# Kernel optimization log

Hardware: AMD Instinct MI355X
Metric: run time of the kernel (lower is better)

The kernel has to match this reference:

```python
import jax, jax.numpy as jnp
import numpy as np

NTOKEN, NINP, NHID, NLAYERS = 33278, 400, 1150, 3


def _lstm_scan(x_seq, h0, c0, Wih, Whh, bih, bhh):
    # x_seq: [T,B,in], h0/c0: [B,H]; PyTorch gate order i,f,g,o
    def step(carry, x):
        h, c = carry
        gates = x @ Wih.T + bih + h @ Whh.T + bhh  # [B,4H]
        i, f, g, o = jnp.split(gates, 4, axis=-1)
        c = jax.nn.sigmoid(f) * c + jax.nn.sigmoid(i) * jnp.tanh(g)
        h = jax.nn.sigmoid(o) * jnp.tanh(c)
        return (h, c), h
    (hT, cT), hs = jax.lax.scan(step, (h0, c0), x_seq)
    return hs, hT, cT


def _causal_attention(hs):
    # hs: [T,B,H]; dot-product attention of h_t over h_{0..t} (causal)
    T = hs.shape[0]
    scores = jnp.einsum('tbh,sbh->bts', hs, hs)  # [B,T,T]
    mask = jnp.tril(jnp.ones((T, T), dtype=bool))
    scores = jnp.where(mask[None, :, :], scores, -1e30)
    attn = jax.nn.softmax(scores, axis=-1)
    return jnp.einsum('bts,sbh->tbh', attn, hs)


def setup_inputs() -> dict:
    key = jax.random.key(0)
    ks = jax.random.split(key, 24)
    T, B = 100, 64
    inp = {
        'input': jax.random.randint(ks[0], (T, B), 0, NTOKEN),
        'input2': jax.random.randint(ks[1], (T, B), 0, NTOKEN),
        'h0': jnp.zeros((1, B, NHID)), 'c0': jnp.zeros((1, B, NHID)),
        'h1': jnp.zeros((1, B, NHID)), 'c1': jnp.zeros((1, B, NHID)),
        'h2': jnp.zeros((1, B, NHID)), 'c2': jnp.zeros((1, B, NHID)),
    }
    inp['emb_W'] = jax.random.uniform(ks[2], (NTOKEN, NINP), minval=-0.1, maxval=0.1)
    in_sizes = [2 * NINP, NHID, NHID]
    for l in range(NLAYERS):
        s = 1.0 / np.sqrt(NHID)
        inp[f'W_ih{l}'] = jax.random.uniform(ks[3 + 4 * l], (4 * NHID, in_sizes[l]), minval=-s, maxval=s)
        inp[f'W_hh{l}'] = jax.random.uniform(ks[4 + 4 * l], (4 * NHID, NHID), minval=-s, maxval=s)
        inp[f'b_ih{l}'] = jax.random.uniform(ks[5 + 4 * l], (4 * NHID,), minval=-s, maxval=s)
        inp[f'b_hh{l}'] = jax.random.uniform(ks[6 + 4 * l], (4 * NHID,), minval=-s, maxval=s)
    inp['dec_W'] = jax.random.uniform(ks[20], (NTOKEN, NHID), minval=-0.1, maxval=0.1)
    inp['dec_b'] = jnp.zeros((NTOKEN,))
    return inp


def reference(input, input2, h0, c0, h1, c1, h2, c2, emb_W,
              W_ih0, W_hh0, b_ih0, b_hh0,
              W_ih1, W_hh1, b_ih1, b_hh1,
              W_ih2, W_hh2, b_ih2, b_hh2,
              dec_W, dec_b):
    # eval mode: all dropouts are identity
    emb = jnp.concatenate([emb_W[input], emb_W[input2]], axis=-1)  # [T,B,2*ninp]
    x = emb
    hcs = [(h0[0], c0[0]), (h1[0], c1[0]), (h2[0], c2[0])]
    params = [(W_ih0, W_hh0, b_ih0, b_hh0), (W_ih1, W_hh1, b_ih1, b_hh1), (W_ih2, W_hh2, b_ih2, b_hh2)]
    for l in range(NLAYERS):
        hs, hT, cT = _lstm_scan(x, hcs[l][0], hcs[l][1], *params[l])
        if l == NLAYERS - 1:
            out = _causal_attention(hs)  # attention only on last layer
        else:
            x = hs
    T, B, H = out.shape
    decoded = out.reshape(T * B, H) @ dec_W.T + dec_b  # [T*B, ntoken]
    return decoded
```

## Files before the change

kernel.cpp:

```cpp
#include <hip/hip_runtime.h>
#include <stdint.h>

typedef unsigned short ushort_t;
typedef __bf16 bf16x8 __attribute__((ext_vector_type(8)));
typedef float f32x4 __attribute__((ext_vector_type(4)));

__device__ __forceinline__ float b2f(ushort_t u) {
  union { unsigned u; float f; } v; v.u = ((unsigned)u) << 16; return v.f;
}
__device__ __forceinline__ ushort_t f2b(float f) {
  union { float f; unsigned u; } v; v.f = f;
  unsigned r = (v.u + 0x7FFFu + ((v.u >> 16) & 1u)) >> 16;
  return (ushort_t)r;
}

__device__ __forceinline__ float sigm(float x)     { return 1.f / (1.f + __expf(-x)); }
__device__ __forceinline__ float tanhfast(float x) { return 1.f - 2.f / (1.f + __expf(2.f * x)); }

__device__ __forceinline__ void store_short_wt(ushort_t* p, ushort_t v) {
  asm volatile("global_store_short %0, %1, off sc0 sc1"
               :: "v"(p), "v"((unsigned)v) : "memory");
}
__device__ __forceinline__ void store_uint_wt(unsigned* p, unsigned v) {
  asm volatile("global_store_dword %0, %1, off sc0 sc1"
               :: "v"(p), "v"(v) : "memory");
}

__device__ __forceinline__ void gload_lds16(const void* g, void* lds) {
  auto l3 = reinterpret_cast<__attribute__((address_space(3))) unsigned*>(
      reinterpret_cast<uintptr_t>(lds));
  __builtin_amdgcn_global_load_lds(reinterpret_cast<const unsigned*>(g), l3, 16, 0, 0);
}

template <bool F32OUT>
__global__ __launch_bounds__(512) void gemm_bt(
    const ushort_t* __restrict__ A, const ushort_t* __restrict__ B,
    void* __restrict__ Cv,
    const float* __restrict__ bias0, const float* __restrict__ bias1,
    int lda, int ldb, long ldc, int Kpad, int N)
{
  __shared__ alignas(16) ushort_t As[256 * 32];
  __shared__ alignas(16) ushort_t Bs[256 * 32];
  const int tid = threadIdx.x;
  const int w = tid >> 6, l = tid & 63;
  const int wr = w >> 2, wc = w & 3;

  unsigned nwg = gridDim.x * gridDim.y;
  unsigned wg = blockIdx.y * gridDim.x + blockIdx.x;
  {
    unsigned q = nwg >> 3, r = nwg & 7u;
    unsigned xcd = wg & 7u, idx = wg >> 3;
    wg = (xcd < r ? xcd * (q + 1) : r * (q + 1) + (xcd - r) * q) + idx;
  }
  const long m0 = (long)(wg % gridDim.x) * 256;
  const long n0 = (long)(wg / gridDim.x) * 256;

  const int lrow = l & 15, hi = l >> 4, lk = hi * 8;

  f32x4 acc[8][4] = {};

  const int c0 = tid, c1 = tid + 512;
  const int r0 = c0 >> 2, g0 = (c0 & 3) * 8;
  const int r1 = c1 >> 2, g1 = (c1 & 3) * 8;

  for (int k0 = 0; k0 < Kpad; k0 += 32) {
    gload_lds16(A + (m0 + r0) * lda + k0 + g0, As + c0 * 8);
    gload_lds16(A + (m0 + r1) * lda + k0 + g1, As + c1 * 8);
    gload_lds16(B + (n0 + r0) * ldb + k0 + g0, Bs + c0 * 8);
    gload_lds16(B + (n0 + r1) * ldb + k0 + g1, Bs + c1 * 8);
    __syncthreads();

    bf16x8 af[8], bfr[4];
#pragma unroll
    for (int mi = 0; mi < 8; mi++)
      af[mi] = *(const bf16x8*)(As + (wr * 128 + mi * 16 + lrow) * 32 + lk);
#pragma unroll
    for (int ni = 0; ni < 4; ni++)
      bfr[ni] = *(const bf16x8*)(Bs + (wc * 64 + ni * 16 + lrow) * 32 + lk);
#pragma unroll
    for (int mi = 0; mi < 8; mi++)
#pragma unroll
      for (int ni = 0; ni < 4; ni++)
        acc[mi][ni] = __builtin_amdgcn_mfma_f32_16x16x32_bf16(af[mi], bfr[ni], acc[mi][ni], 0, 0, 0);
    __syncthreads();
  }

  const int rbase = hi * 4;
#pragma unroll
  for (int ni = 0; ni < 4; ni++) {
    int gcol = (int)n0 + wc * 64 + ni * 16 + lrow;
    if (gcol < N) {
      float badd = 0.f;
      if (bias0) badd += bias0[gcol];
      if (bias1) badd += bias1[gcol];
#pragma unroll
      for (int mi = 0; mi < 8; mi++) {
#pragma unroll
        for (int r = 0; r < 4; r++) {
          long grow = m0 + wr * 128 + mi * 16 + rbase + r;
          float v = acc[mi][ni][r] + badd;
          if (F32OUT) ((float*)Cv)[grow * ldc + gcol] = v;
          else        ((ushort_t*)Cv)[grow * ldc + gcol] = f2b(v);
        }
      }
    }
  }
}

__global__ __launch_bounds__(256) void lstm_layer(
    ushort_t* __restrict__ hs,
    const ushort_t* __restrict__ G,
    const ushort_t* __restrict__ Whh,
    const float* __restrict__ c_in,
    unsigned* __restrict__ flags)
{
  extern __shared__ ushort_t Bsh[];
  const int tid = threadIdx.x;
  const int w = tid >> 6, l = tid & 63;
  const int us = blockIdx.x;
  const int lrow = l & 15, hi = l >> 4, lk = hi * 8;
  const int u = us * 16 + lrow;
  const int usafe = (u < 1150) ? u : 0;
  const int row0 = w * 16 + hi * 4;
  const int x7 = lrow & 7;
  const int start = us >> 1;

  for (int ci = tid; ci < 9216; ci += 256) {
    int gate = ci / 2304;
    int rem  = ci - gate * 2304;
    int row  = rem / 144;
    int c    = rem - row * 144;
    bf16x8 v = *(const bf16x8*)(Whh + ((long)(gate * 1150 + us * 16 + row)) * 1152 + c * 8);
    *(bf16x8*)(Bsh + (((gate * 16 + row) * 144) + (c ^ (row & 7))) * 8) = v;
  }
  const ushort_t* Bg0 = Bsh + ((0 * 16 + lrow) * 144) * 8;
  const ushort_t* Bg1 = Bsh + ((1 * 16 + lrow) * 144) * 8;
  const ushort_t* Bg2 = Bsh + ((2 * 16 + lrow) * 144) * 8;
  const ushort_t* Bg3 = Bsh + ((3 * 16 + lrow) * 144) * 8;

  f32x4 cc = {};
  if (u < 1150) {
#pragma unroll
    for (int r = 0; r < 4; ++r) cc[r] = c_in[(row0 + r) * 1150 + u];
  }
  __syncthreads();

  const int s1 = l, s2 = 64 + (l & 7);

  for (int t = 0; t < 100; ++t) {
    ushort_t gvv[16];
    {
      const ushort_t* gp = G + ((long)t * 64 + row0) * 4608 + usafe;
#pragma unroll
      for (int r = 0; r < 4; ++r)
#pragma unroll
        for (int g = 0; g < 4; ++g)
          gvv[r * 4 + g] = gp[(long)r * 4608 + g * 1150];
    }

    if (t > 0) {
      if (w == 0) {
        const unsigned tt = (unsigned)t;
        unsigned f1 = (s1 == us) ? tt :
            __hip_atomic_load(flags + (s1 << 5), __ATOMIC_RELAXED, __HIP_MEMORY_SCOPE_AGENT);
        unsigned f2 = (s2 == us) ? tt :
            __hip_atomic_load(flags + (s2 << 5), __ATOMIC_RELAXED, __HIP_MEMORY_SCOPE_AGENT);
        unsigned long long p1 = __ballot(f1 >= tt);
        unsigned long long p2 = __ballot(f2 >= tt);
        while ((p1 & p2) != ~0ull) {
          __builtin_amdgcn_s_sleep(8);
          if (!((p1 >> l) & 1))
            f1 = __hip_atomic_load(flags + (s1 << 5), __ATOMIC_RELAXED, __HIP_MEMORY_SCOPE_AGENT);
          if (!((p2 >> l) & 1))
            f2 = __hip_atomic_load(flags + (s2 << 5), __ATOMIC_RELAXED, __HIP_MEMORY_SCOPE_AGENT);
          p1 = __ballot(f1 >= tt);
          p2 = __ballot(f2 >= tt);
        }
      }
      __syncthreads();
      asm volatile("" ::: "memory");
    }

    const ushort_t* hp = hs + (long)t * 73728 + (long)(w * 16 + lrow) * 1152 + lk;
    f32x4 a0 = {}, a1 = {}, a2 = {}, a3 = {};
#pragma unroll 4
    for (int i = 0; i < 36; ++i) {
      int kc = start + i; if (kc >= 36) kc -= 36;
      bf16x8 a = *(const bf16x8*)(hp + kc * 32);
      int pc8 = ((kc * 4 + hi) ^ x7) * 8;
      a0 = __builtin_amdgcn_mfma_f32_16x16x32_bf16(a, *(const bf16x8*)(Bg0 + pc8), a0, 0, 0, 0);
      a1 = __builtin_amdgcn_mfma_f32_16x16x32_bf16(a, *(const bf16x8*)(Bg1 + pc8), a1, 0, 0, 0);
      a2 = __builtin_amdgcn_mfma_f32_16x16x32_bf16(a, *(const bf16x8*)(Bg2 + pc8), a2, 0, 0, 0);
      a3 = __builtin_amdgcn_mfma_f32_16x16x32_bf16(a, *(const bf16x8*)(Bg3 + pc8), a3, 0, 0, 0);
    }

    if (u < 1150) {
#pragma unroll
      for (int r = 0; r < 4; ++r) {
        float iv = a0[r] + b2f(gvv[r * 4 + 0]);
        float fv = a1[r] + b2f(gvv[r * 4 + 1]);
        float gg = a2[r] + b2f(gvv[r * 4 + 2]);
        float ov = a3[r] + b2f(gvv[r * 4 + 3]);
        float cn = sigm(fv) * cc[r] + sigm(iv) * tanhfast(gg);
        cc[r] = cn;
        float hv = sigm(ov) * tanhfast(cn);
        store_short_wt(hs + (long)(t + 1) * 73728 + (long)(row0 + r) * 1152 + u, f2b(hv));
      }
    }

    if (t != 99) {
      asm volatile("s_waitcnt vmcnt(0)" ::: "memory");
      __syncthreads();
      if (tid == 0) store_uint_wt(flags + (us << 5), (unsigned)(t + 1));
    }
  }
}

__global__ __launch_bounds__(256) void attn_kernel(
    const ushort_t* __restrict__ hs2,
    ushort_t* __restrict__ outp)
{
  __shared__ float qf[1152];
  __shared__ float sc[104];
  __shared__ float sinv;
  const int rowi = blockIdx.x;
  const int t = rowi >> 6, b = rowi & 63;
  const int tid = threadIdx.x;
  const int w = tid >> 6, l = tid & 63;

  const ushort_t* q = hs2 + (long)rowi * 1152;
  for (int c = tid; c < 1150; c += 256) qf[c] = b2f(q[c]);
  __syncthreads();

  for (int s = w; s <= t; s += 4) {
    const ushort_t* k = hs2 + (long)(s * 64 + b) * 1152;
    float p = 0.f;
    for (int h = l; h < 1150; h += 64) p += qf[h] * b2f(k[h]);
    for (int off = 32; off; off >>= 1) p += __shfl_down(p, off);
    if (l == 0) sc[s] = p;
  }
  __syncthreads();

  if (w == 0) {
    float m = -1e30f;
    for (int s = l; s <= t; s += 64) m = fmaxf(m, sc[s]);
    for (int off = 32; off; off >>= 1) m = fmaxf(m, __shfl_down(m, off));
    m = __shfl(m, 0);
    float sum = 0.f;
    for (int s = l; s <= t; s += 64) { float e = __expf(sc[s] - m); sc[s] = e; sum += e; }
    for (int off = 32; off; off >>= 1) sum += __shfl_down(sum, off);
    if (l == 0) sinv = 1.f / sum;
  }
  __syncthreads();

  const float si = sinv;
  for (int h = tid; h < 1150; h += 256) {
    float a = 0.f;
    for (int s = 0; s <= t; s++) a += sc[s] * b2f(hs2[(long)(s * 64 + b) * 1152 + h]);
    outp[(long)rowi * 1152 + h] = f2b(a * si);
  }
  if (tid < 2) outp[(long)rowi * 1152 + 1150 + tid] = 0;
}

__global__ void embed_kernel(const int* __restrict__ in1, const int* __restrict__ in2,
                             const float* __restrict__ emb, ushort_t* __restrict__ x0)
{
  int rowi = blockIdx.x;
  int l = threadIdx.x;
  long r1 = (long)in1[rowi] * 400, r2 = (long)in2[rowi] * 400;
  ushort_t* d = x0 + (long)rowi * 800;
  for (int c = l; c < 800; c += 64)
    d[c] = f2b(c < 400 ? emb[r1 + c] : emb[r2 + c - 400]);
}

__global__ void pad_convert(const float* __restrict__ in, ushort_t* __restrict__ out,
                            int R, int Cin, int total, int Cp)
{
  int idx = blockIdx.x * 256 + threadIdx.x;
  if (idx >= total) return;
  int r = idx / Cp, c = idx - r * Cp;
  float v = (r < R && c < Cin) ? in[(long)r * Cin + c] : 0.f;
  out[idx] = f2b(v);
}

__global__ void init_state(const float* __restrict__ h_in,
                           ushort_t* __restrict__ hs, unsigned* __restrict__ flags)
{
  int idx = blockIdx.x * 256 + threadIdx.x;
  if (idx < 72 * 32) flags[idx] = 0u;
  if (idx < 64 * 1152) {
    int b = idx / 1152, c = idx - b * 1152;
    hs[idx] = (c < 1150) ? f2b(h_in[b * 1150 + c]) : (ushort_t)0;
  }
  if (idx < 100 * 128) {
    int t = idx >> 7, r = idx & 127, b = r >> 1, k = r & 1;
    hs[(long)(t + 1) * 73728 + b * 1152 + 1150 + k] = 0;
  }
}

extern "C" void kernel_launch(void* const* d_in, const int* in_sizes, int n_in,
                              void* d_out, int out_size, void* d_ws, size_t ws_size,
                              hipStream_t stream) {
  (void)in_sizes; (void)n_in; (void)out_size; (void)ws_size;
  const int* input  = (const int*)d_in[0];
  const int* input2 = (const int*)d_in[1];
  const float* h_in[3] = {(const float*)d_in[2], (const float*)d_in[4], (const float*)d_in[6]};
  const float* c_in[3] = {(const float*)d_in[3], (const float*)d_in[5], (const float*)d_in[7]};
  const float* emb_W = (const float*)d_in[8];
  const float* W_ih[3] = {(const float*)d_in[9],  (const float*)d_in[13], (const float*)d_in[17]};
  const float* W_hh[3] = {(const float*)d_in[10], (const float*)d_in[14], (const float*)d_in[18]};
  const float* b_ih[3] = {(const float*)d_in[11], (const float*)d_in[15], (const float*)d_in[19]};
  const float* b_hh[3] = {(const float*)d_in[12], (const float*)d_in[16], (const float*)d_in[20]};
  const float* dec_W = (const float*)d_in[21];
  const float* dec_b = (const float*)d_in[22];
  float* out = (float*)d_out;

  hipFuncSetAttribute((const void*)lstm_layer,
                      hipFuncAttributeMaxDynamicSharedMemorySize, 147456);

  char* base = (char*)d_ws;
  size_t off = 0;
  auto walloc = [&](size_t bytes) { char* r = base + off; off += (bytes + 255) & ~(size_t)255; return r; };
  ushort_t* decWp = (ushort_t*)walloc(33280ull * 1152 * 2);
  ushort_t* attnB = (ushort_t*)walloc(6400ull * 1152 * 2);
  unsigned* flags = (unsigned*)walloc(72 * 128 + 256);

  char* ob = (char*)d_out;
  ushort_t* G   = (ushort_t*)(ob + 0);
  ushort_t* x0  = (ushort_t*)(ob + 58982400);
  ushort_t* Wp  = (ushort_t*)(ob + 69222400);
  ushort_t* Whp = (ushort_t*)(ob + 79839232);
  ushort_t* hsA = (ushort_t*)(ob + 90456064);
  ushort_t* hsB = (ushort_t*)(ob + 105349120);

  embed_kernel<<<6400, 64, 0, stream>>>(input, input2, emb_W, x0);

  ushort_t* hcur[3] = {hsA, hsB, hsA};
  const ushort_t* X = x0;
  int lda = 800, Kp = 800;
  for (int lyr = 0; lyr < 3; lyr++) {
    if (lyr == 0) {
      int tot = 4608 * 800;
      pad_convert<<<(tot + 255) / 256, 256, 0, stream>>>(W_ih[0], Wp, 4600, 800, tot, 800);
    } else {
      int tot = 4608 * 1152;
      pad_convert<<<(tot + 255) / 256, 256, 0, stream>>>(W_ih[lyr], Wp, 4600, 1150, tot, 1152);
    }
    {
      int tot = 4608 * 1152;
      pad_convert<<<(tot + 255) / 256, 256, 0, stream>>>(W_hh[lyr], Whp, 4600, 1150, tot, 1152);
    }
    gemm_bt<false><<<dim3(25, 18), 512, 0, stream>>>(X, Wp, (void*)G, b_ih[lyr], b_hh[lyr],
                                                     lda, Kp, 4608L, Kp, 4600);
    init_state<<<288, 256, 0, stream>>>(h_in[lyr], hcur[lyr], flags);
    lstm_layer<<<72, 256, 147456, stream>>>(hcur[lyr], G, Whp, c_in[lyr], flags);
    X = hcur[lyr] + 73728;
    lda = 1152; Kp = 1152;
  }

  attn_kernel<<<6400, 256, 0, stream>>>(hsA + 73728, attnB);

  {
    int tot = 33280 * 1152;
    pad_convert<<<(tot + 255) / 256, 256, 0, stream>>>(dec_W, decWp, 33278, 1150, tot, 1152);
  }

  gemm_bt<true><<<dim3(25, 130), 512, 0, stream>>>(attnB, decWp, (void*)out, dec_b, nullptr,
                                                   1152, 1152, 33278L, 1152, 33278);
}
```

Measured before the change: 3.997 ms.

## Fuse three LSTM layers into one wavefront-pipelined persistent kernel

Replaces three sequential per-layer LSTM launches (each preceded by an input-projection GEMM) with a single persistent kernel of 216 blocks, 72 per layer. Layers 1 and 2 compute the input projection inline by streaming W_ih rows from global memory, and each waits on per-timestep flags from the layer below, so the three layers run as a diagonal wavefront. This removes the two layer-1/2 input GEMMs and the serialization between layers. In exchange it doubles the MFMA work per step for upper layers, reads uncached W_ih from global/L2 every step, and needs all 216 blocks co-resident with 144KB LDS each to avoid deadlock.

```diff
diff --git a/kernel.cpp b/kernel.cpp
--- a/kernel.cpp
+++ b/kernel.cpp
@@ -107,23 +107,44 @@
   }
 }
 
-__global__ __launch_bounds__(256) void lstm_layer(
-    ushort_t* __restrict__ hs,
-    const ushort_t* __restrict__ G,
-    const ushort_t* __restrict__ Whh,
-    const float* __restrict__ c_in,
+__global__ __launch_bounds__(256) void lstm_fused3(
+    ushort_t* __restrict__ hs0, ushort_t* __restrict__ hs1, ushort_t* __restrict__ hs2,
+    const ushort_t* __restrict__ G0,
+    const ushort_t* __restrict__ Whp0, const ushort_t* __restrict__ Whp1,
+    const ushort_t* __restrict__ Whp2,
+    const ushort_t* __restrict__ Wip1, const ushort_t* __restrict__ Wip2,
+    const float* __restrict__ c0, const float* __restrict__ c1, const float* __restrict__ c2,
+    const float* __restrict__ bi1, const float* __restrict__ bh1,
+    const float* __restrict__ bi2, const float* __restrict__ bh2,
     unsigned* __restrict__ flags)
 {
   extern __shared__ ushort_t Bsh[];
   const int tid = threadIdx.x;
   const int w = tid >> 6, l = tid & 63;
-  const int us = blockIdx.x;
+  const int L  = blockIdx.x / 72;
+  const int us = blockIdx.x % 72;
   const int lrow = l & 15, hi = l >> 4, lk = hi * 8;
   const int u = us * 16 + lrow;
   const int usafe = (u < 1150) ? u : 0;
   const int row0 = w * 16 + hi * 4;
   const int x7 = lrow & 7;
   const int start = us >> 1;
+
+  ushort_t* hsL = (L == 0) ? hs0 : (L == 1) ? hs1 : hs2;
+  const ushort_t* hsP = (L == 1) ? hs0 : hs1;
+  const ushort_t* Whh = (L == 0) ? Whp0 : (L == 1) ? Whp1 : Whp2;
+  const ushort_t* Wih = (L == 1) ? Wip1 : Wip2;
+  const float* cin = (L == 0) ? c0 : (L == 1) ? c1 : c2;
+  unsigned* fown  = flags + L * 2304;
+  unsigned* fprev = flags + (L - 1) * 2304;
+
+  float bias4[4] = {0.f, 0.f, 0.f, 0.f};
+  if (L > 0) {
+    const float* bi = (L == 1) ? bi1 : bi2;
+    const float* bh = (L == 1) ? bh1 : bh2;
+#pragma unroll
+    for (int g = 0; g < 4; ++g) bias4[g] = bi[g * 1150 + usafe] + bh[g * 1150 + usafe];
+  }
 
   for (int ci = tid; ci < 9216; ci += 256) {
     int gate = ci / 2304;
@@ -138,19 +159,42 @@
   const ushort_t* Bg2 = Bsh + ((2 * 16 + lrow) * 144) * 8;
   const ushort_t* Bg3 = Bsh + ((3 * 16 + lrow) * 144) * 8;
 
+  const ushort_t* wi0 = Wih + ((long)(0 * 1150 + us * 16 + lrow)) * 1152 + lk;
+  const ushort_t* wi1 = Wih + ((long)(1 * 1150 + us * 16 + lrow)) * 1152 + lk;
+  const ushort_t* wi2 = Wih + ((long)(2 * 1150 + us * 16 + lrow)) * 1152 + lk;
+  const ushort_t* wi3 = Wih + ((long)(3 * 1150 + us * 16 + lrow)) * 1152 + lk;
+
   f32x4 cc = {};
   if (u < 1150) {
 #pragma unroll
-    for (int r = 0; r < 4; ++r) cc[r] = c_in[(row0 + r) * 1150 + u];
+    for (int r = 0; r < 4; ++r) cc[r] = cin[(row0 + r) * 1150 + u];
   }
   __syncthreads();
 
   const int s1 = l, s2 = 64 + (l & 7);
+
+  auto waitarr = [&](unsigned* f, unsigned tt, bool exempt) {
+    unsigned f1 = (exempt && s1 == us) ? tt :
+        __hip_atomic_load(f + (s1 << 5), __ATOMIC_RELAXED, __HIP_MEMORY_SCOPE_AGENT);
+    unsigned f2 = (exempt && s2 == us) ? tt :
+        __hip_atomic_load(f + (s2 << 5), __ATOMIC_RELAXED, __HIP_MEMORY_SCOPE_AGENT);
+    unsigned long long p1 = __ballot(f1 >= tt);
+    unsigned long long p2 = __ballot(f2 >= tt);
+    while ((p1 & p2) != ~0ull) {
+      __builtin_amdgcn_s_sleep(8);
+      if (!((p1 >> l) & 1))
+        f1 = __hip_atomic_load(f + (s1 << 5), __ATOMIC_RELAXED, __HIP_MEMORY_SCOPE_AGENT);
+      if (!((p2 >> l) & 1))
+        f2 = __hip_atomic_load(f + (s2 << 5), __ATOMIC_RELAXED, __HIP_MEMORY_SCOPE_AGENT);
+      p1 = __ballot(f1 >= tt);
+      p2 = __ballot(f2 >= tt);
+    }
+  };
 
   for (int t = 0; t < 100; ++t) {
     ushort_t gvv[16];
-    {
-      const ushort_t* gp = G + ((long)t * 64 + row0) * 4608 + usafe;
+    if (L == 0) {
+      const ushort_t* gp = G0 + ((long)t * 64 + row0) * 4608 + usafe;
 #pragma unroll
       for (int r = 0; r < 4; ++r)
 #pragma unroll
@@ -158,61 +202,74 @@
           gvv[r * 4 + g] = gp[(long)r * 4608 + g * 1150];
     }
 
-    if (t > 0) {
-      if (w == 0) {
-        const unsigned tt = (unsigned)t;
-        unsigned f1 = (s1 == us) ? tt :
-            __hip_atomic_load(flags + (s1 << 5), __ATOMIC_RELAXED, __HIP_MEMORY_SCOPE_AGENT);
-        unsigned f2 = (s2 == us) ? tt :
-            __hip_atomic_load(flags + (s2 << 5), __ATOMIC_RELAXED, __HIP_MEMORY_SCOPE_AGENT);
-        unsigned long long p1 = __ballot(f1 >= tt);
-        unsigned long long p2 = __ballot(f2 >= tt);
-        while ((p1 & p2) != ~0ull) {
-          __builtin_amdgcn_s_sleep(8);
-          if (!((p1 >> l) & 1))
-            f1 = __hip_atomic_load(flags + (s1 << 5), __ATOMIC_RELAXED, __HIP_MEMORY_SCOPE_AGENT);
-          if (!((p2 >> l) & 1))
-            f2 = __hip_atomic_load(flags + (s2 << 5), __ATOMIC_RELAXED, __HIP_MEMORY_SCOPE_AGENT);
-          p1 = __ballot(f1 >= tt);
-          p2 = __ballot(f2 >= tt);
-        }
-      }
+    if (w == 0) {
+      if (t > 0) waitarr(fown, (unsigned)t, true);
+      if (L > 0) waitarr(fprev, (unsigned)(t + 1), false);
+    }
+    if (t > 0 || L > 0) {
       __syncthreads();
       asm volatile("" ::: "memory");
     }
 
-    const ushort_t* hp = hs + (long)t * 73728 + (long)(w * 16 + lrow) * 1152 + lk;
+    const ushort_t* hp = hsL + (long)t * 73728 + (long)(w * 16 + lrow) * 1152 + lk;
     f32x4 a0 = {}, a1 = {}, a2 = {}, a3 = {};
+
+    if (L == 0) {
 #pragma unroll 4
-    for (int i = 0; i < 36; ++i) {
-      int kc = start + i; if (kc >= 36) kc -= 36;
-      bf16x8 a = *(const bf16x8*)(hp + kc * 32);
-      int pc8 = ((kc * 4 + hi) ^ x7) * 8;
-      a0 = __builtin_amdgcn_mfma_f32_16x16x32_bf16(a, *(const bf16x8*)(Bg0 + pc8), a0, 0, 0, 0);
-      a1 = __builtin_amdgcn_mfma_f32_16x16x32_bf16(a, *(const bf16x8*)(Bg1 + pc8), a1, 0, 0, 0);
-      a2 = __builtin_amdgcn_mfma_f32_16x16x32_bf16(a, *(const bf16x8*)(Bg2 + pc8), a2, 0, 0, 0);
-      a3 = __builtin_amdgcn_mfma_f32_16x16x32_bf16(a, *(const bf16x8*)(Bg3 + pc8), a3, 0, 0, 0);
+      for (int i = 0; i < 36; ++i) {
+        int kc = start + i; if (kc >= 36) kc -= 36;
+        bf16x8 a = *(const bf16x8*)(hp + kc * 32);
+        int pc8 = ((kc * 4 + hi) ^ x7) * 8;
+        a0 = __builtin_amdgcn_mfma_f32_16x16x32_bf16(a, *(const bf16x8*)(Bg0 + pc8), a0, 0, 0, 0);
+        a1 = __builtin_amdgcn_mfma_f32_16x16x32_bf16(a, *(const bf16x8*)(Bg1 + pc8), a1, 0, 0, 0);
+        a2 = __builtin_amdgcn_mfma_f32_16x16x32_bf16(a, *(const bf16x8*)(Bg2 + pc8), a2, 0, 0, 0);
+        a3 = __builtin_amdgcn_mfma_f32_16x16x32_bf16(a, *(const bf16x8*)(Bg3 + pc8), a3, 0, 0, 0);
+      }
+    } else {
+      const ushort_t* xp = hsP + (long)(t + 1) * 73728 + (long)(w * 16 + lrow) * 1152 + lk;
+#pragma unroll 2
+      for (int i = 0; i < 36; ++i) {
+        int kc = start + i; if (kc >= 36) kc -= 36;
+        int koff = kc * 32;
+        bf16x8 ah = *(const bf16x8*)(hp + koff);
+        bf16x8 ax = *(const bf16x8*)(xp + koff);
+        int pc8 = ((kc * 4 + hi) ^ x7) * 8;
+        a0 = __builtin_amdgcn_mfma_f32_16x16x32_bf16(ah, *(const bf16x8*)(Bg0 + pc8), a0, 0, 0, 0);
+        a1 = __builtin_amdgcn_mfma_f32_16x16x32_bf16(ah, *(const bf16x8*)(Bg1 + pc8), a1, 0, 0, 0);
+        a2 = __builtin_amdgcn_mfma_f32_16x16x32_bf16(ah, *(const bf16x8*)(Bg2 + pc8), a2, 0, 0, 0);
+        a3 = __builtin_amdgcn_mfma_f32_16x16x32_bf16(ah, *(const bf16x8*)(Bg3 + pc8), a3, 0, 0, 0);
+        a0 = __builtin_amdgcn_mfma_f32_16x16x32_bf16(ax, *(const bf16x8*)(wi0 + koff), a0, 0, 0, 0);
+        a1 = __builtin_amdgcn_mfma_f32_16x16x32_bf16(ax, *(const bf16x8*)(wi1 + koff), a1, 0, 0, 0);
+        a2 = __builtin_amdgcn_mfma_f32_16x16x32_bf16(ax, *(const bf16x8*)(wi2 + koff), a2, 0, 0, 0);
+        a3 = __builtin_amdgcn_mfma_f32_16x16x32_bf16(ax, *(const bf16x8*)(wi3 + koff), a3, 0, 0, 0);
+      }
     }
 
     if (u < 1150) {
 #pragma unroll
       for (int r = 0; r < 4; ++r) {
-        float iv = a0[r] + b2f(gvv[r * 4 + 0]);
-        float fv = a1[r] + b2f(gvv[r * 4 + 1]);
-        float gg = a2[r] + b2f(gvv[r * 4 + 2]);
-        float ov = a3[r] + b2f(gvv[r * 4 + 3]);
+        float iv, fv, gg, ov;
+        if (L == 0) {
+          iv = a0[r] + b2f(gvv[r * 4 + 0]);
+          fv = a1[r] + b2f(gvv[r * 4 + 1]);
+          gg = a2[r] + b2f(gvv[r * 4 + 2]);
+          ov = a3[r] + b2f(gvv[r * 4 + 3]);
+        } else {
+          iv = a0[r] + bias4[0];
+          fv = a1[r] + bias4[1];
+          gg = a2[r] + bias4[2];
+          ov = a3[r] + bias4[3];
+        }
         float cn = sigm(fv) * cc[r] + sigm(iv) * tanhfast(gg);
         cc[r] = cn;
         float hv = sigm(ov) * tanhfast(cn);
-        store_short_wt(hs + (long)(t + 1) * 73728 + (long)(row0 + r) * 1152 + u, f2b(hv));
+        store_short_wt(hsL + (long)(t + 1) * 73728 + (long)(row0 + r) * 1152 + u, f2b(hv));
       }
     }
 
-    if (t != 99) {
-      asm volatile("s_waitcnt vmcnt(0)" ::: "memory");
-      __syncthreads();
-      if (tid == 0) store_uint_wt(flags + (us << 5), (unsigned)(t + 1));
-    }
+    asm volatile("s_waitcnt vmcnt(0)" ::: "memory");
+    __syncthreads();
+    if (tid == 0) store_uint_wt(fown + (us << 5), (unsigned)(t + 1));
   }
 }
 
@@ -283,11 +340,17 @@
   out[idx] = f2b(v);
 }
 
-__global__ void init_state(const float* __restrict__ h_in,
-                           ushort_t* __restrict__ hs, unsigned* __restrict__ flags)
-{
+__global__ void init_state3(const float* __restrict__ h0, const float* __restrict__ h1,
+                            const float* __restrict__ h2,
+                            ushort_t* __restrict__ hs0, ushort_t* __restrict__ hs1,
+                            ushort_t* __restrict__ hs2,
+                            unsigned* __restrict__ flags)
+{
+  int L = blockIdx.y;
+  const float* h_in = (L == 0) ? h0 : (L == 1) ? h1 : h2;
+  ushort_t* hs = (L == 0) ? hs0 : (L == 1) ? hs1 : hs2;
   int idx = blockIdx.x * 256 + threadIdx.x;
-  if (idx < 72 * 32) flags[idx] = 0u;
+  if (idx < 72 * 32) flags[L * 2304 + idx] = 0u;
   if (idx < 64 * 1152) {
     int b = idx / 1152, c = idx - b * 1152;
     hs[idx] = (c < 1150) ? f2b(h_in[b * 1150 + c]) : (ushort_t)0;
@@ -315,7 +378,7 @@
   const float* dec_b = (const float*)d_in[22];
   float* out = (float*)d_out;
 
-  hipFuncSetAttribute((const void*)lstm_layer,
+  hipFuncSetAttribute((const void*)lstm_fused3,
                       hipFuncAttributeMaxDynamicSharedMemorySize, 147456);
 
   char* base = (char*)d_ws;
@@ -323,42 +386,47 @@
   auto walloc = [&](size_t bytes) { char* r = base + off; off += (bytes + 255) & ~(size_t)255; return r; };
   ushort_t* decWp = (ushort_t*)walloc(33280ull * 1152 * 2);
   ushort_t* attnB = (ushort_t*)walloc(6400ull * 1152 * 2);
-  unsigned* flags = (unsigned*)walloc(72 * 128 + 256);
+  unsigned* flags = (unsigned*)walloc(3 * 72 * 128 + 256);
 
   char* ob = (char*)d_out;
-  ushort_t* G   = (ushort_t*)(ob + 0);
-  ushort_t* x0  = (ushort_t*)(ob + 58982400);
-  ushort_t* Wp  = (ushort_t*)(ob + 69222400);
-  ushort_t* Whp = (ushort_t*)(ob + 79839232);
-  ushort_t* hsA = (ushort_t*)(ob + 90456064);
-  ushort_t* hsB = (ushort_t*)(ob + 105349120);
+  ushort_t* G0   = (ushort_t*)(ob + 0);
+  ushort_t* x0   = (ushort_t*)(ob + 58982400);
+  ushort_t* Wp0  = (ushort_t*)(ob + 69222400);
+  ushort_t* Whp0 = (ushort_t*)(ob + 76595200);
+  ushort_t* Whp1 = (ushort_t*)(ob + 87212032);
+  ushort_t* Whp2 = (ushort_t*)(ob + 97828864);
+  ushort_t* Wip1 = (ushort_t*)(ob + 108445696);
+  ushort_t* Wip2 = (ushort_t*)(ob + 119062528);
+  ushort_t* hsL0 = (ushort_t*)(ob + 129679360);
+  ushort_t* hsL1 = (ushort_t*)(ob + 144572416);
+  ushort_t* hsL2 = (ushort_t*)(ob + 159465472);
 
   embed_kernel<<<6400, 64, 0, stream>>>(input, input2, emb_W, x0);
 
-  ushort_t* hcur[3] = {hsA, hsB, hsA};
-  const ushort_t* X = x0;
-  int lda = 800, Kp = 800;
-  for (int lyr = 0; lyr < 3; lyr++) {
-    if (lyr == 0) {
-      int tot = 4608 * 800;
-      pad_convert<<<(tot + 255) / 256, 256, 0, stream>>>(W_ih[0], Wp, 4600, 800, tot, 800);
-    } else {
-      int tot = 4608 * 1152;
-      pad_convert<<<(tot + 255) / 256, 256, 0, stream>>>(W_ih[lyr], Wp, 4600, 1150, tot, 1152);
-    }
-    {
-      int tot = 4608 * 1152;
-      pad_convert<<<(tot + 255) / 256, 256, 0, stream>>>(W_hh[lyr], Whp, 4600, 1150, tot, 1152);
-    }
-    gemm_bt<false><<<dim3(25, 18), 512, 0, stream>>>(X, Wp, (void*)G, b_ih[lyr], b_hh[lyr],
-                                                     lda, Kp, 4608L, Kp, 4600);
-    init_state<<<288, 256, 0, stream>>>(h_in[lyr], hcur[lyr], flags);
-    lstm_layer<<<72, 256, 147456, stream>>>(hcur[lyr], G, Whp, c_in[lyr], flags);
-    X = hcur[lyr] + 73728;
-    lda = 1152; Kp = 1152;
-  }
-
-  attn_kernel<<<6400, 256, 0, stream>>>(hsA + 73728, attnB);
+  {
+    int tot = 4608 * 800;
+    pad_convert<<<(tot + 255) / 256, 256, 0, stream>>>(W_ih[0], Wp0, 4600, 800, tot, 800);
+  }
+  {
+    int tot = 4608 * 1152;
+    pad_convert<<<(tot + 255) / 256, 256, 0, stream>>>(W_hh[0], Whp0, 4600, 1150, tot, 1152);
+    pad_convert<<<(tot + 255) / 256, 256, 0, stream>>>(W_hh[1], Whp1, 4600, 1150, tot, 1152);
+    pad_convert<<<(tot + 255) / 256, 256, 0, stream>>>(W_hh[2], Whp2, 4600, 1150, tot, 1152);
+    pad_convert<<<(tot + 255) / 256, 256, 0, stream>>>(W_ih[1], Wip1, 4600, 1150, tot, 1152);
+    pad_convert<<<(tot + 255) / 256, 256, 0, stream>>>(W_ih[2], Wip2, 4600, 1150, tot, 1152);
+  }
+
+  gemm_bt<false><<<dim3(25, 18), 512, 0, stream>>>(x0, Wp0, (void*)G0, b_ih[0], b_hh[0],
+                                                   800, 800, 4608L, 800, 4600);
+
+  init_state3<<<dim3(288, 3), 256, 0, stream>>>(h_in[0], h_in[1], h_in[2],
+                                                hsL0, hsL1, hsL2, flags);
+
+  lstm_fused3<<<216, 256, 147456, stream>>>(
+      hsL0, hsL1, hsL2, G0, Whp0, Whp1, Whp2, Wip1, Wip2,
+      c_in[0], c_in[1], c_in[2], b_ih[1], b_hh[1], b_ih[2], b_hh[2], flags);
+
+  attn_kernel<<<6400, 256, 0, stream>>>(hsL2 + 73728, attnB);
 
   {
     int tot = 33280 * 1152;
```

New measurement: 4.314 ms. 1.08x slower.
